# Kernel tuning notes

Hardware: AMD Instinct MI355X
Metric: run time of the kernel (lower is better)

Reference implementation:

```python
import jax, jax.numpy as jnp
import numpy as np

B, N, D, U = 8, 4096, 128, 1024


def setup_inputs() -> dict:
    key = jax.random.key(0)
    kx, kw = jax.random.split(key)
    x = jax.random.normal(kx, (B, N, D), dtype=jnp.float32)
    # learned kernel, shape (dims, units) as in build()
    w = jax.random.normal(kw, (D, U), dtype=jnp.float32)
    return {"x": x, "w": w}


def reference(x, w):
    # Squared Euclidean distance from every point x[b,n,:] to every prototype
    # column w[:,u]: sum_d (x[b,n,d] - w[d,u])^2.
    # work is a single GEMM instead of materializing a [B,N,D,U] tensor.
    x2 = jnp.sum(x * x, axis=-1, keepdims=True)        # [B, N, 1]
    w2 = jnp.sum(w * w, axis=0)                        # [U]
    xw = jnp.einsum("bnd,du->bnu", x, w)               # [B, N, U]
    a = x2 + w2 - 2.0 * xw                             # [B, N, U]
    # inverted=False, activation=None -> return raw squared distances
    return a
```

## Files before the change

### kernel.cpp

```cpp
#include <hip/hip_runtime.h>

#define M_TOT 32768
#define K_DIM 128
#define U_TOT 1024

#define BM 128
#define BN 128
#define BK 32

typedef short s16x8 __attribute__((ext_vector_type(8)));
typedef float f32x4 __attribute__((ext_vector_type(4)));

__device__ inline unsigned int f2bf(float f) {
    union { float f; unsigned int u; } v; v.f = f;
    unsigned int r = v.u + 0x7FFFu + ((v.u >> 16) & 1u);
    return r >> 16;
}

__device__ inline void async_load16(const void* g, void* l) {
    __builtin_amdgcn_global_load_lds((const __attribute__((address_space(1))) void*)g,
                                     (__attribute__((address_space(3))) void*)l,
                                     16, 0, 0);
}

__global__ __launch_bounds__(256) void prep_kernel(
    const float* __restrict__ x, const float* __restrict__ w,
    unsigned int* __restrict__ xb, unsigned int* __restrict__ wt,
    float* __restrict__ x2, float* __restrict__ w2)
{
    const int lane = threadIdx.x & 63;
    const int gw = (blockIdx.x << 2) + (threadIdx.x >> 6);
    if (gw < M_TOT) {
        const float2 v = ((const float2*)(x + (size_t)gw * K_DIM))[lane];
        float s = v.x * v.x + v.y * v.y;
        #pragma unroll
        for (int off = 32; off; off >>= 1) s += __shfl_xor(s, off);
        xb[gw * 64 + lane] = f2bf(v.x) | (f2bf(v.y) << 16);
        if (lane == 0) x2[gw] = s;
    } else if (gw < M_TOT + U_TOT) {
        const int u = gw - M_TOT;
        const float a = w[(size_t)(2 * lane) * U_TOT + u];
        const float b = w[(size_t)(2 * lane + 1) * U_TOT + u];
        float s = a * a + b * b;
        #pragma unroll
        for (int off = 32; off; off >>= 1) s += __shfl_xor(s, off);
        wt[u * 64 + lane] = f2bf(a) | (f2bf(b) << 16);
        if (lane == 0) w2[u] = s;
    }
}

__global__ __launch_bounds__(256) void gemm_kernel(
    const unsigned short* __restrict__ xb, const unsigned short* __restrict__ wt,
    const float* __restrict__ x2, const float* __restrict__ w2,
    float* __restrict__ out)
{
    __shared__ __align__(16) unsigned short As[BM * BK];
    __shared__ __align__(16) unsigned short Bs[BN * BK];

    const int tid = threadIdx.x;
    const int wv = tid >> 6;
    const int lane = tid & 63;
    const int m0 = (int)(blockIdx.x >> 3) * BM;
    const int u0 = (int)(blockIdx.x & 7) * BN;
    const int wm = (wv & 1) * 64;
    const int wn = (wv >> 1) * 64;
    const int col = lane & 15;
    const int quad = lane >> 4;
    const int srow = lane >> 2;
    const int sch = (lane & 3) * 8;

    f32x4 acc[4][4] = {};

    #pragma unroll
    for (int kt = 0; kt < 4; ++kt) {
        const int k0 = kt * BK;
        #pragma unroll
        for (int i = 0; i < 2; ++i) {
            const int rb = (wv * 2 + i) * 16;
            async_load16(xb + (size_t)(m0 + rb + srow) * K_DIM + k0 + sch, &As[rb * BK]);
            async_load16(wt + (size_t)(u0 + rb + srow) * K_DIM + k0 + sch, &Bs[rb * BK]);
        }
        __syncthreads();

        s16x8 af[4], bfr[4];
        #pragma unroll
        for (int t = 0; t < 4; ++t) {
            af[t]  = *(const s16x8*)&As[(wm + t * 16 + col) * BK + quad * 8];
            bfr[t] = *(const s16x8*)&Bs[(wn + t * 16 + col) * BK + quad * 8];
        }
        #pragma unroll
        for (int a = 0; a < 4; ++a)
            #pragma unroll
            for (int b = 0; b < 4; ++b)
                acc[a][b] = __builtin_amdgcn_mfma_f32_16x16x32_bf16(af[a], bfr[b], acc[a][b], 0, 0, 0);
        __syncthreads();
    }

    const int orow = quad * 4;
    #pragma unroll
    for (int a = 0; a < 4; ++a) {
        const int mb = m0 + wm + a * 16 + orow;
        float xs[4];
        #pragma unroll
        for (int r = 0; r < 4; ++r) xs[r] = x2[mb + r];
        #pragma unroll
        for (int b = 0; b < 4; ++b) {
            const int u = u0 + wn + b * 16 + col;
            const float wsq = w2[u];
            float* op = out + (size_t)mb * U_TOT + u;
            #pragma unroll
            for (int r = 0; r < 4; ++r)
                op[(size_t)r * U_TOT] = xs[r] + wsq - 2.0f * acc[a][b][r];
        }
    }
}

__global__ __launch_bounds__(256) void fallback_kernel(
    const float* __restrict__ x, const float* __restrict__ w,
    float* __restrict__ out)
{
    __shared__ float xrow[K_DIM];
    const int m = blockIdx.x;
    const int tid = threadIdx.x;
    if (tid < K_DIM) xrow[tid] = x[(size_t)m * K_DIM + tid];
    __syncthreads();
    float x2 = 0.f;
    #pragma unroll
    for (int k = 0; k < K_DIM; ++k) x2 += xrow[k] * xrow[k];
    #pragma unroll
    for (int uu = 0; uu < 4; ++uu) {
        const int u = uu * 256 + tid;
        float dot = 0.f, w2 = 0.f;
        for (int k = 0; k < K_DIM; ++k) {
            const float wv = w[(size_t)k * U_TOT + u];
            dot += xrow[k] * wv;
            w2 += wv * wv;
        }
        out[(size_t)m * U_TOT + u] = x2 + w2 - 2.0f * dot;
    }
}

extern "C" void kernel_launch(void* const* d_in, const int* in_sizes, int n_in,
                              void* d_out, int out_size, void* d_ws, size_t ws_size,
                              hipStream_t stream) {
    const float* x = (const float*)d_in[0];
    const float* w = (const float*)d_in[1];
    float* out = (float*)d_out;

    const size_t need = (size_t)M_TOT * K_DIM * 2 + (size_t)U_TOT * K_DIM * 2
                      + (size_t)M_TOT * 4 + (size_t)U_TOT * 4;
    if (ws_size < need) {
        fallback_kernel<<<M_TOT, 256, 0, stream>>>(x, w, out);
        return;
    }

    unsigned short* xb = (unsigned short*)d_ws;
    unsigned short* wt = xb + (size_t)M_TOT * K_DIM;
    float* x2 = (float*)(wt + (size_t)U_TOT * K_DIM);
    float* w2 = x2 + M_TOT;

    prep_kernel<<<(M_TOT + U_TOT) / 4, 256, 0, stream>>>(x, w, (unsigned int*)xb,
                                                         (unsigned int*)wt, x2, w2);
    gemm_kernel<<<(M_TOT / BM) * (U_TOT / BN), 256, 0, stream>>>(xb, wt, x2, w2, out);
}
```

Baseline: 161.2 us.

## Load GEMM fragments directly from global memory and store float4 rows

Removes the LDS staging and the block-wide barriers in the GEMM. Each wave now reads its bf16 fragments straight from global memory, counting on L2/L1 for reuse across waves. The MFMA operands are swapped so each lane holds four consecutive output columns, which allows one 16-byte float4 store per tile instead of four scattered scalar stores. The trade-off is more redundant global and L2 traffic, since waves no longer share tiles through LDS, plus less coalesced fragment loads.

```diff
diff --git a/kernel.cpp b/kernel.cpp
--- a/kernel.cpp
+++ b/kernel.cpp
@@ -3,10 +3,6 @@
 #define M_TOT 32768
 #define K_DIM 128
 #define U_TOT 1024
-
-#define BM 128
-#define BN 128
-#define BK 32
 
 typedef short s16x8 __attribute__((ext_vector_type(8)));
 typedef float f32x4 __attribute__((ext_vector_type(4)));
@@ -15,12 +11,6 @@
     union { float f; unsigned int u; } v; v.f = f;
     unsigned int r = v.u + 0x7FFFu + ((v.u >> 16) & 1u);
     return r >> 16;
-}
-
-__device__ inline void async_load16(const void* g, void* l) {
-    __builtin_amdgcn_global_load_lds((const __attribute__((address_space(1))) void*)g,
-                                     (__attribute__((address_space(3))) void*)l,
-                                     16, 0, 0);
 }
 
 __global__ __launch_bounds__(256) void prep_kernel(
@@ -54,63 +44,56 @@
     const float* __restrict__ x2, const float* __restrict__ w2,
     float* __restrict__ out)
 {
-    __shared__ __align__(16) unsigned short As[BM * BK];
-    __shared__ __align__(16) unsigned short Bs[BN * BK];
-
     const int tid = threadIdx.x;
     const int wv = tid >> 6;
     const int lane = tid & 63;
-    const int m0 = (int)(blockIdx.x >> 3) * BM;
-    const int u0 = (int)(blockIdx.x & 7) * BN;
+    const int col = lane & 15;
+    const int quad = lane >> 4;
+    const int m0 = (int)(blockIdx.x >> 3) * 128;
+    const int u0 = (int)(blockIdx.x & 7) * 128;
     const int wm = (wv & 1) * 64;
     const int wn = (wv >> 1) * 64;
-    const int col = lane & 15;
-    const int quad = lane >> 4;
-    const int srow = lane >> 2;
-    const int sch = (lane & 3) * 8;
+
+    const unsigned short* arow = xb + (size_t)(m0 + wm + col) * K_DIM;
+    const unsigned short* brow = wt + (size_t)(u0 + wn + col) * K_DIM;
 
     f32x4 acc[4][4] = {};
 
-    #pragma unroll
-    for (int kt = 0; kt < 4; ++kt) {
-        const int k0 = kt * BK;
-        #pragma unroll
-        for (int i = 0; i < 2; ++i) {
-            const int rb = (wv * 2 + i) * 16;
-            async_load16(xb + (size_t)(m0 + rb + srow) * K_DIM + k0 + sch, &As[rb * BK]);
-            async_load16(wt + (size_t)(u0 + rb + srow) * K_DIM + k0 + sch, &Bs[rb * BK]);
-        }
-        __syncthreads();
-
-        s16x8 af[4], bfr[4];
+    #pragma unroll 1
+    for (int kc = 0; kc < 4; ++kc) {
+        const int ko = kc * 32 + quad * 8;
+        s16x8 af[4], bf[4];
         #pragma unroll
         for (int t = 0; t < 4; ++t) {
-            af[t]  = *(const s16x8*)&As[(wm + t * 16 + col) * BK + quad * 8];
-            bfr[t] = *(const s16x8*)&Bs[(wn + t * 16 + col) * BK + quad * 8];
+            af[t] = *(const s16x8*)(arow + t * 16 * K_DIM + ko);
+            bf[t] = *(const s16x8*)(brow + t * 16 * K_DIM + ko);
         }
         #pragma unroll
         for (int a = 0; a < 4; ++a)
             #pragma unroll
             for (int b = 0; b < 4; ++b)
-                acc[a][b] = __builtin_amdgcn_mfma_f32_16x16x32_bf16(af[a], bfr[b], acc[a][b], 0, 0, 0);
-        __syncthreads();
+                acc[a][b] = __builtin_amdgcn_mfma_f32_16x16x32_bf16(bf[b], af[a], acc[a][b], 0, 0, 0);
     }
 
-    const int orow = quad * 4;
+    float xs[4];
+    #pragma unroll
+    for (int a = 0; a < 4; ++a) xs[a] = x2[m0 + wm + a * 16 + col];
+    float4 ws4[4];
+    #pragma unroll
+    for (int b = 0; b < 4; ++b) ws4[b] = *(const float4*)&w2[u0 + wn + b * 16 + quad * 4];
+
     #pragma unroll
     for (int a = 0; a < 4; ++a) {
-        const int mb = m0 + wm + a * 16 + orow;
-        float xs[4];
-        #pragma unroll
-        for (int r = 0; r < 4; ++r) xs[r] = x2[mb + r];
+        const size_t mrow = (size_t)(m0 + wm + a * 16 + col) * U_TOT;
         #pragma unroll
         for (int b = 0; b < 4; ++b) {
-            const int u = u0 + wn + b * 16 + col;
-            const float wsq = w2[u];
-            float* op = out + (size_t)mb * U_TOT + u;
-            #pragma unroll
-            for (int r = 0; r < 4; ++r)
-                op[(size_t)r * U_TOT] = xs[r] + wsq - 2.0f * acc[a][b][r];
+            const int ub = u0 + wn + b * 16 + quad * 4;
+            float4 o;
+            o.x = xs[a] + ws4[b].x - 2.0f * acc[a][b][0];
+            o.y = xs[a] + ws4[b].y - 2.0f * acc[a][b][1];
+            o.z = xs[a] + ws4[b].z - 2.0f * acc[a][b][2];
+            o.w = xs[a] + ws4[b].w - 2.0f * acc[a][b][3];
+            *(float4*)&out[mrow + ub] = o;
         }
     }
 }
@@ -161,5 +144,5 @@
 
     prep_kernel<<<(M_TOT + U_TOT) / 4, 256, 0, stream>>>(x, w, (unsigned int*)xb,
                                                          (unsigned int*)wt, x2, w2);
-    gemm_kernel<<<(M_TOT / BM) * (U_TOT / BN), 256, 0, stream>>>(xb, wt, x2, w2, out);
+    gemm_kernel<<<(M_TOT / 128) * (U_TOT / 128), 256, 0, stream>>>(xb, wt, x2, w2, out);
 }
```

New measurement: 182.6 us. 13.3% more time.
